# Kernel tuning notes

Hardware: AMD Instinct MI355X
Metric: run time of the kernel (lower is better)

Reference implementation:

```python
import jax, jax.numpy as jnp
import numpy as np

N_NODES = 1_000_000
FEAT_DIM = 128
EMBED_DIM = 128
BATCH = 8192
NUM_SAMPLE = 10
N_LABELED = 16384
EPS = 1e-6
TEMP = 5.0


def setup_inputs() -> dict:
    key = jax.random.key(0)
    ks = jax.random.split(key, 8)
    return {
        "nodes": jax.random.randint(ks[0], (BATCH,), 0, N_NODES),
        "neigh_idx": jax.random.randint(ks[1], (BATCH, NUM_SAMPLE), 0, N_NODES),
        "pos_index": jax.random.randint(ks[2], (N_LABELED,), 0, N_NODES),
        "neg_index": jax.random.randint(ks[3], (N_LABELED,), 0, N_NODES),
        "features": jax.random.normal(ks[4], (N_NODES, FEAT_DIM), dtype=jnp.float32),
        "weight": jax.random.normal(ks[5], (EMBED_DIM, 2 * FEAT_DIM), dtype=jnp.float32) * (1.0 / np.sqrt(2 * FEAT_DIM)),
        "pos_vector": jax.random.normal(ks[6], (1, FEAT_DIM), dtype=jnp.float32),
        "neg_vector": jax.random.normal(ks[7], (1, FEAT_DIM), dtype=jnp.float32),
    }


def _update_vector(vec, x):
    # torch CosineSimilarity(dim=1, eps=1e-6) between [1,D] vec and [M,D] x -> [M]
    dot = jnp.einsum("md,d->m", x, vec[0])
    nv = jnp.maximum(jnp.linalg.norm(vec[0]), EPS)
    nx = jnp.maximum(jnp.linalg.norm(x, axis=1), EPS)
    cos = dot / (nv * nx)
    w = jax.nn.softmax(cos / TEMP)[None, :]  # softmax_with_temperature, t=5
    return jax.lax.stop_gradient(w @ x)  # [1, D], detached in torch


def reference(nodes, neigh_idx, pos_index, neg_index, features, weight, pos_vector, neg_vector):
    # Mean aggregator over sampled neighbors: [B, S, D] -> [B, D]
    neigh_feats = jnp.mean(features[neigh_idx], axis=1)
    # update_label_vector side computation (running vectors already initialized)
    new_pos = _update_vector(pos_vector, features[pos_index])
    new_neg = _update_vector(neg_vector, features[neg_index])
    # self features gather + concat + weight.mm + relu
    self_feats = features[nodes]                      # [B, D]
    combined = jnp.concatenate([self_feats, neigh_feats], axis=1)  # [B, 2D]
    out = jax.nn.relu(weight @ combined.T)            # [E, B]
    return out, new_pos, new_neg
```

## Files before the change

### kernel.cpp

```cpp
#include <hip/hip_runtime.h>
#include <hip/hip_bf16.h>
#include <stdint.h>

#define BATCH 8192
#define NSAMP 10
#define FDIM 128
#define K2 256
#define EDIM 128
#define NLAB 16384
#define EPSF 1e-6f

#define CPAD 264

typedef __bf16 bf16x8 __attribute__((ext_vector_type(8)));
typedef float f32x4 __attribute__((ext_vector_type(4)));

struct alignas(8) bfx4 { __hip_bfloat16 a, b, c, d; };

#define NPART 1024

__global__ __launch_bounds__(256) void fusedA(
    const int* __restrict__ nodes, const int* __restrict__ neigh,
    const int* __restrict__ pos_idx, const int* __restrict__ neg_idx,
    const float* __restrict__ feats,
    const float* __restrict__ pos_vec, const float* __restrict__ neg_vec,
    const float* __restrict__ W,
    float* __restrict__ partial,
    float* __restrict__ out)
{
    __shared__ __hip_bfloat16 comb[32][CPAD];

    int blk  = blockIdx.x;
    int tid  = threadIdx.x;
    int lane = tid & 63;
    int wv   = tid >> 6;
    int hl   = lane & 31;
    int half = lane >> 5;
    int hw   = wv * 2 + half;

    if (blk < 256) {
        int n0 = blk * 32;

        for (int rr = 0; rr < 4; ++rr) {
            int lr  = hw * 4 + rr;
            int row = n0 + lr;
            int ids[NSAMP + 1];
            ids[0] = nodes[row];
            #pragma unroll
            for (int j = 0; j < NSAMP; ++j) ids[1 + j] = neigh[row * NSAMP + j];

            f32x4 s = ((const f32x4*)(feats + (size_t)ids[0] * FDIM))[hl];
            f32x4 acc = {0.f, 0.f, 0.f, 0.f};
            #pragma unroll
            for (int j = 0; j < NSAMP; ++j) {
                f32x4 v = ((const f32x4*)(feats + (size_t)ids[1 + j] * FDIM))[hl];
                acc += v;
            }
            acc *= 0.1f;

            bfx4 t;
            t.a = __float2bfloat16(s[0]); t.b = __float2bfloat16(s[1]);
            t.c = __float2bfloat16(s[2]); t.d = __float2bfloat16(s[3]);
            *(bfx4*)(&comb[lr][4 * hl]) = t;
            t.a = __float2bfloat16(acc[0]); t.b = __float2bfloat16(acc[1]);
            t.c = __float2bfloat16(acc[2]); t.d = __float2bfloat16(acc[3]);
            *(bfx4*)(&comb[lr][FDIM + 4 * hl]) = t;
        }
        __syncthreads();

        int llo = lane & 15, lhi = lane >> 4;
        int m0 = wv * 32;

        f32x4 acc[2][2];
        #pragma unroll
        for (int i = 0; i < 2; ++i)
            #pragma unroll
            for (int j = 0; j < 2; ++j) { f32x4 z = {0.f,0.f,0.f,0.f}; acc[i][j] = z; }

        #pragma unroll
        for (int k0 = 0; k0 < K2; k0 += 32) {
            bf16x8 a[2], b[2];
            #pragma unroll
            for (int mi = 0; mi < 2; ++mi) {
                const float* wp = W + (size_t)(m0 + 16*mi + llo) * K2 + k0 + lhi*8;
                f32x4 w0 = ((const f32x4*)wp)[0];
                f32x4 w1 = ((const f32x4*)wp)[1];
                bf16x8 af;
                af[0] = (__bf16)w0[0]; af[1] = (__bf16)w0[1];
                af[2] = (__bf16)w0[2]; af[3] = (__bf16)w0[3];
                af[4] = (__bf16)w1[0]; af[5] = (__bf16)w1[1];
                af[6] = (__bf16)w1[2]; af[7] = (__bf16)w1[3];
                a[mi] = af;
            }
            #pragma unroll
            for (int ni = 0; ni < 2; ++ni) {
                const uint4* p = (const uint4*)(&comb[16*ni + llo][k0 + lhi*8]);
                b[ni] = __builtin_bit_cast(bf16x8, *p);
            }
            #pragma unroll
            for (int mi = 0; mi < 2; ++mi)
                #pragma unroll
                for (int ni = 0; ni < 2; ++ni)
                    acc[mi][ni] = __builtin_amdgcn_mfma_f32_16x16x32_bf16(a[mi], b[ni], acc[mi][ni], 0, 0, 0);
        }

        #pragma unroll
        for (int mi = 0; mi < 2; ++mi)
            #pragma unroll
            for (int ni = 0; ni < 2; ++ni)
                #pragma unroll
                for (int j = 0; j < 4; ++j) {
                    int row = m0 + 16*mi + lhi*4 + j;
                    int col = n0 + 16*ni + llo;
                    out[(size_t)row * BATCH + col] = fmaxf(acc[mi][ni][j], 0.f);
                }
    } else {
        int b     = blk - 256;
        int sel   = b >> 8;
        int inner = b & 255;
        int wid   = inner * 4 + wv;
        const int*   idx = sel ? neg_idx : pos_idx;
        const float* vec = sel ? neg_vec : pos_vec;

        f32x4 v4 = ((const f32x4*)vec)[hl];
        float pv = v4[0]*v4[0] + v4[1]*v4[1] + v4[2]*v4[2] + v4[3]*v4[3];
        #pragma unroll
        for (int off = 16; off; off >>= 1) pv += __shfl_xor(pv, off);
        float inv5nv = 1.f / (5.f * fmaxf(sqrtf(pv), EPSF));

        f32x4 a4 = {0.f, 0.f, 0.f, 0.f};
        float es = 0.f;

        #pragma unroll
        for (int g = 0; g < 2; ++g) {
            int base = wid * 16 + g * 8;
            int id[4];
            #pragma unroll
            for (int it = 0; it < 4; ++it) id[it] = idx[base + 2 * it + half];

            f32x4 x[4];
            #pragma unroll
            for (int it = 0; it < 4; ++it)
                x[it] = ((const f32x4*)(feats + (size_t)id[it] * FDIM))[hl];

            float d[4], nx[4];
            #pragma unroll
            for (int it = 0; it < 4; ++it) {
                d[it]  = x[it][0]*v4[0] + x[it][1]*v4[1] + x[it][2]*v4[2] + x[it][3]*v4[3];
                nx[it] = x[it][0]*x[it][0] + x[it][1]*x[it][1] + x[it][2]*x[it][2] + x[it][3]*x[it][3];
            }
            #pragma unroll
            for (int off = 16; off; off >>= 1) {
                #pragma unroll
                for (int it = 0; it < 4; ++it) {
                    d[it]  += __shfl_xor(d[it], off);
                    nx[it] += __shfl_xor(nx[it], off);
                }
            }
            #pragma unroll
            for (int it = 0; it < 4; ++it) {
                float n2 = fmaxf(sqrtf(nx[it]), EPSF);
                float e = __expf(d[it] * inv5nv / n2);
                es += e;
                a4 += e * x[it];
            }
        }

        #pragma unroll
        for (int c = 0; c < 4; ++c) a4[c] += __shfl_xor(a4[c], 32);
        es += __shfl_xor(es, 32);
        float* pw = partial + ((size_t)sel * NPART + wid) * 132;
        if (lane < 32) ((f32x4*)pw)[lane] = a4;
        if (lane == 0) pw[128] = es;
    }
}

__global__ __launch_bounds__(256) void stage2k(
    const float* __restrict__ partial, float* __restrict__ outv)
{
    int lane = threadIdx.x & 63;
    int wv   = threadIdx.x >> 6;
    int widx = blockIdx.x * 4 + wv;
    int sel = widx >> 7;
    int d   = widx & 127;
    const float* p = partial + (size_t)sel * NPART * 132;
    float s = 0.f, es = 0.f;
    for (int w = lane; w < NPART; w += 64) {
        s  += p[w * 132 + d];
        es += p[w * 132 + 128];
    }
    #pragma unroll
    for (int off = 32; off; off >>= 1) {
        s  += __shfl_xor(s, off);
        es += __shfl_xor(es, off);
    }
    if (lane == 0) outv[sel * 128 + d] = s / es;
}

extern "C" void kernel_launch(void* const* d_in, const int* in_sizes, int n_in,
                              void* d_out, int out_size, void* d_ws, size_t ws_size,
                              hipStream_t stream) {
    const int*   nodes = (const int*)d_in[0];
    const int*   neigh = (const int*)d_in[1];
    const int*   pos_i = (const int*)d_in[2];
    const int*   neg_i = (const int*)d_in[3];
    const float* feats = (const float*)d_in[4];
    const float* W     = (const float*)d_in[5];
    const float* pvec  = (const float*)d_in[6];
    const float* nvec  = (const float*)d_in[7];
    float* out = (float*)d_out;

    float* partial = (float*)d_ws;

    hipLaunchKernelGGL(fusedA, dim3(768), dim3(256), 0, stream,
                       nodes, neigh, pos_i, neg_i, feats, pvec, nvec, W, partial, out);
    hipLaunchKernelGGL(stage2k, dim3(64), dim3(256), 0, stream,
                       partial, out + 1048576);
}
```

Baseline: 27.18 us.

## Halve GEMM tile to 16 nodes and interleave gather/softmax blocks

The aggregation+GEMM blocks now handle 16 nodes instead of 32, so the grid grows to 512 GEMM blocks. They alternate with the 512 label-vector softmax blocks by block parity instead of coming first. This is meant to raise parallelism for the latency-bound gathers and to spread the two kinds of work evenly across CUs. In exchange, each GEMM block reloads and converts the full weight matrix for half as many nodes, doubling total W traffic and conversion work.

```diff
diff --git a/kernel.cpp b/kernel.cpp
--- a/kernel.cpp
+++ b/kernel.cpp
@@ -28,7 +28,7 @@
     float* __restrict__ partial,
     float* __restrict__ out)
 {
-    __shared__ __hip_bfloat16 comb[32][CPAD];
+    __shared__ __hip_bfloat16 comb[16][CPAD];
 
     int blk  = blockIdx.x;
     int tid  = threadIdx.x;
@@ -38,11 +38,13 @@
     int half = lane >> 5;
     int hw   = wv * 2 + half;
 
-    if (blk < 256) {
-        int n0 = blk * 32;
-
-        for (int rr = 0; rr < 4; ++rr) {
-            int lr  = hw * 4 + rr;
+    if ((blk & 1) == 0) {
+        int g  = blk >> 1;
+        int n0 = g * 16;
+
+        #pragma unroll
+        for (int rr = 0; rr < 2; ++rr) {
+            int lr  = hw * 2 + rr;
             int row = n0 + lr;
             int ids[NSAMP + 1];
             ids[0] = nodes[row];
@@ -71,15 +73,13 @@
         int llo = lane & 15, lhi = lane >> 4;
         int m0 = wv * 32;
 
-        f32x4 acc[2][2];
-        #pragma unroll
-        for (int i = 0; i < 2; ++i)
-            #pragma unroll
-            for (int j = 0; j < 2; ++j) { f32x4 z = {0.f,0.f,0.f,0.f}; acc[i][j] = z; }
+        f32x4 acc[2];
+        #pragma unroll
+        for (int i = 0; i < 2; ++i) { f32x4 z = {0.f,0.f,0.f,0.f}; acc[i] = z; }
 
         #pragma unroll
         for (int k0 = 0; k0 < K2; k0 += 32) {
-            bf16x8 a[2], b[2];
+            bf16x8 a[2], b;
             #pragma unroll
             for (int mi = 0; mi < 2; ++mi) {
                 const float* wp = W + (size_t)(m0 + 16*mi + llo) * K2 + k0 + lhi*8;
@@ -92,30 +92,22 @@
                 af[6] = (__bf16)w1[2]; af[7] = (__bf16)w1[3];
                 a[mi] = af;
             }
-            #pragma unroll
-            for (int ni = 0; ni < 2; ++ni) {
-                const uint4* p = (const uint4*)(&comb[16*ni + llo][k0 + lhi*8]);
-                b[ni] = __builtin_bit_cast(bf16x8, *p);
-            }
+            b = __builtin_bit_cast(bf16x8, *(const uint4*)(&comb[llo][k0 + lhi*8]));
             #pragma unroll
             for (int mi = 0; mi < 2; ++mi)
-                #pragma unroll
-                for (int ni = 0; ni < 2; ++ni)
-                    acc[mi][ni] = __builtin_amdgcn_mfma_f32_16x16x32_bf16(a[mi], b[ni], acc[mi][ni], 0, 0, 0);
+                acc[mi] = __builtin_amdgcn_mfma_f32_16x16x32_bf16(a[mi], b, acc[mi], 0, 0, 0);
         }
 
         #pragma unroll
         for (int mi = 0; mi < 2; ++mi)
             #pragma unroll
-            for (int ni = 0; ni < 2; ++ni)
-                #pragma unroll
-                for (int j = 0; j < 4; ++j) {
-                    int row = m0 + 16*mi + lhi*4 + j;
-                    int col = n0 + 16*ni + llo;
-                    out[(size_t)row * BATCH + col] = fmaxf(acc[mi][ni][j], 0.f);
-                }
+            for (int j = 0; j < 4; ++j) {
+                int row = m0 + 16*mi + lhi*4 + j;
+                int col = n0 + llo;
+                out[(size_t)row * BATCH + col] = fmaxf(acc[mi][j], 0.f);
+            }
     } else {
-        int b     = blk - 256;
+        int b     = blk >> 1;
         int sel   = b >> 8;
         int inner = b & 255;
         int wid   = inner * 4 + wv;
@@ -212,7 +204,7 @@
 
     float* partial = (float*)d_ws;
 
-    hipLaunchKernelGGL(fusedA, dim3(768), dim3(256), 0, stream,
+    hipLaunchKernelGGL(fusedA, dim3(1024), dim3(256), 0, stream,
                        nodes, neigh, pos_i, neg_i, feats, pvec, nvec, W, partial, out);
     hipLaunchKernelGGL(stage2k, dim3(64), dim3(256), 0, stream,
                        partial, out + 1048576);
```

Result: slower. 36.40 us (+33.9%).
